# Optimization experiments

Hardware: AMD Instinct MI355X
Metric: run time of the kernel (lower is better)

## Reference

```python
import jax, jax.numpy as jnp
import numpy as np
from functools import partial

B, S, T = 256, 256, 32      # batch, encoder seq len, decoder max len
H = 512                     # hidden_dim
E = 128                     # encoder token embed dim
ED = 32                     # decoder action/target embed dim (LSTM input = 2*ED)
V = 1000                    # encoder vocab
A = 8                       # num_actions
NT = 80                     # num_targets


def lstm_cell(x, h, c, Wi, Wh, b):
    # PyTorch gate order: i, f, g, o
    z = x @ Wi.T + h @ Wh.T + b
    i, f, g, o = jnp.split(z, 4, axis=-1)
    c = jax.nn.sigmoid(f) * c + jax.nn.sigmoid(i) * jnp.tanh(g)
    h = jax.nn.sigmoid(o) * jnp.tanh(c)
    return h, c


def setup_inputs() -> dict:
    key = jax.random.key(0)
    ks = jax.random.split(key, 16)
    s = 0.05
    rn = lambda k, shp: (jax.random.normal(k, shp, dtype=jnp.float32) * s)
    return {
        "encoder_input": jax.random.randint(ks[0], (B, S), 0, V),
        "decoder_target": jax.random.randint(ks[1], (B, T, 2), 0, A),
        "enc_embed": rn(ks[2], (V, E)),
        "Wi_e": rn(ks[3], (4 * H, E)),
        "Wh_e": rn(ks[4], (4 * H, H)),
        "b_e": jnp.zeros((4 * H,), jnp.float32),
        "act_emb": rn(ks[5], (A, ED)),
        "tgt_emb": rn(ks[6], (NT, ED)),
        "Wi_d": rn(ks[7], (4 * H, 2 * ED)),
        "Wh_d": rn(ks[8], (4 * H, H)),
        "b_d": jnp.zeros((4 * H,), jnp.float32),
        "W_a": rn(ks[9], (A, H)),
        "b_a": jnp.zeros((A,), jnp.float32),
        "W_t": rn(ks[10], (NT, H)),
        "b_t": jnp.zeros((NT,), jnp.float32),
        "Wf": rn(ks[11], (1, 2 * H)),   # additive-attention scorer Linear(2H, 1)
        "bf": jnp.zeros((1,), jnp.float32),
    }


def reference(encoder_input, decoder_target, enc_embed, Wi_e, Wh_e, b_e,
              act_emb, tgt_emb, Wi_d, Wh_d, b_d, W_a, b_a, W_t, b_t, Wf, bf):
    # ---- encoder: embedding + single-layer LSTM over S steps ----
    x = enc_embed[encoder_input]          # [B, S, E]
    h0 = jnp.zeros((B, H), jnp.float32)
    c0 = jnp.zeros((B, H), jnp.float32)

    def enc_step(carry, xt):
        h, c = carry
        h, c = lstm_cell(xt, h, c, Wi_e, Wh_e, b_e)
        return (h, c), h

    (h, c), enc_out = jax.lax.scan(enc_step, (h0, c0), x.transpose(1, 0, 2))
    # enc_out: [S, B, H] (seq-major, matches torch LSTM output layout)

    # fc(concat(enc_i, dec_h)) == enc_i @ We + dec_h @ Wd + bf -> precompute enc part
    We = Wf[0, :H]                        # [H]
    Wd = Wf[0, H:]                        # [H]
    enc_score = jnp.einsum('sbh,h->sb', enc_out, We)   # [S, B]

    dec_in0 = jnp.zeros((B, 2), jnp.int32)

    def dec_step(carry, _):
        h, c, inp = carry
        xt = jnp.concatenate([act_emb[inp[:, 0]], tgt_emb[inp[:, 1]]], axis=-1)  # [B, 2*ED]
        h, c = lstm_cell(xt, h, c, Wi_d, Wh_d, b_d)
        scores = enc_score + h @ Wd + bf[0]            # [S, B]
        w = jax.nn.softmax(scores, axis=0)             # softmax over seq (dim=0)
        ctx = jnp.einsum('sbh,sb->bh', enc_out, w)     # weighted hidden state
        pa = ctx @ W_a.T + b_a                         # [B, A]
        pt = ctx @ W_t.T + b_t                         # [B, NT]
        inp = jnp.stack([jnp.argmax(pa, axis=1), jnp.argmax(pt, axis=1)],
                        axis=-1).astype(jnp.int32)     # greedy feedback (no TF)
        return (h, c, inp), (pa, pt)

    _, (pa_seq, pt_seq) = jax.lax.scan(dec_step, (h, c, dec_in0), None, length=T)
    action_outputs = pa_seq.transpose(1, 0, 2)   # [B, T, A]
    target_outputs = pt_seq.transpose(1, 0, 2)   # [B, T, NT]
    return action_outputs, target_outputs
```

## Files before the change

kernel.cpp:

```cpp
#include <hip/hip_runtime.h>
#include <hip/hip_fp16.h>


#define Sv 256
#define Tv 32
#define Hv 512
#define KT 16
#define LDSA 520
#define GM 16

#define ENC_KEY 0x7FFF7FFFu

typedef _Float16 half8 __attribute__((ext_vector_type(8)));
typedef __attribute__((ext_vector_type(4))) float f32x4;
typedef __attribute__((ext_vector_type(4))) unsigned uint4v;

__device__ __forceinline__ float sigm(float x) { return 1.0f / (1.0f + __expf(-x)); }
__device__ __forceinline__ float tanh_fast(float x) {
  x = fminf(15.f, fmaxf(-15.f, x));
  float e = __expf(2.f * x);
  return (e - 1.f) / (e + 1.f);
}

__device__ __forceinline__ uint4v ld_b128_sys(const void* p) {
  uint4v r;
  asm volatile("global_load_dwordx4 %0, %1, off sc0 sc1" : "=v"(r) : "v"(p));
  return r;
}

__device__ __forceinline__ unsigned umin4(uint4v r) {
  unsigned a = r[0] < r[1] ? r[0] : r[1];
  unsigned b = r[2] < r[3] ? r[2] : r[3];
  return a < b ? a : b;
}

__global__ __launch_bounds__(256)
void build_P(const float* __restrict__ embed, const float* __restrict__ Wi,
             const float* __restrict__ be, float* __restrict__ P)
{
  __shared__ float ev[4][128];
  const int tid = threadIdx.x;
  const int v0  = blockIdx.x * 4;
#pragma unroll
  for (int i = 0; i < 2; ++i) {
    int e = tid + i * 256;
    ev[e >> 7][e & 127] = embed[(v0 + (e >> 7)) * 128 + (e & 127)];
  }
  __syncthreads();
#pragma unroll 1
  for (int cc = 0; cc < 8; ++cc) {
    int n = cc * 256 + tid;
    float b = be[n];
    float a0 = b, a1 = b, a2 = b, a3 = b;
    const f32x4* w = (const f32x4*)(Wi + n * 128);
#pragma unroll
    for (int k4 = 0; k4 < 32; ++k4) {
      f32x4 wv = w[k4];
#pragma unroll
      for (int j = 0; j < 4; ++j) {
        float wj = wv[j];
        int k = k4 * 4 + j;
        a0 += wj * ev[0][k]; a1 += wj * ev[1][k];
        a2 += wj * ev[2][k]; a3 += wj * ev[3][k];
      }
    }
    P[(size_t)(v0 + 0) * 2048 + n] = a0;
    P[(size_t)(v0 + 1) * 2048 + n] = a1;
    P[(size_t)(v0 + 2) * 2048 + n] = a2;
    P[(size_t)(v0 + 3) * 2048 + n] = a3;
  }
}

__global__ __launch_bounds__(256, 1)
void lstm_enc(const int* __restrict__ enc_in, const float* __restrict__ P,
              const float* __restrict__ Wh, __half* __restrict__ enc_out)
{
  __shared__ __attribute__((aligned(16))) _Float16 Ah[GM][LDSA];
  __shared__ float zbuf[4][GM][37];

  const int tid  = threadIdx.x;
  const int wg   = blockIdx.x;
  const int g    = wg & 15;
  const int cb   = wg >> 4;
  const int wave = tid >> 6;
  const int lane = tid & 63;
  const int m16  = lane & 15;
  const int qd   = lane >> 4;

  half8 wf[KT][2];
#pragma unroll
  for (int kt = 0; kt < KT; ++kt) {
#pragma unroll
    for (int nt = 0; nt < 2; ++nt) {
      int n  = wave * 512 + cb * 32 + nt * 16 + m16;
      int k0 = kt * 32 + qd * 8;
      const float* src = Wh + (size_t)n * Hv + k0;
      f32x4 f0 = *(const f32x4*)(src);
      f32x4 f1 = *(const f32x4*)(src + 4);
      half8 w;
      w[0] = (_Float16)f0[0]; w[1] = (_Float16)f0[1];
      w[2] = (_Float16)f0[2]; w[3] = (_Float16)f0[3];
      w[4] = (_Float16)f1[0]; w[5] = (_Float16)f1[1];
      w[6] = (_Float16)f1[2]; w[7] = (_Float16)f1[3];
      wf[kt][nt] = w;
    }
  }

  const int gr = tid >> 4;
  const int gj = (tid & 15) * 2;
  float c0 = 0.f, c1 = 0.f;

  const int r0   = qd * 4;
  const int ncol = wave * 512 + cb * 32 + m16;
  float px0[4], px1[4];
#pragma unroll
  for (int rr = 0; rr < 4; ++rr) {
    int tk  = enc_in[(g * GM + r0 + rr) * Sv + 0];
    px0[rr] = P[(size_t)tk * 2048 + ncol];
    px1[rr] = P[(size_t)tk * 2048 + ncol + 16];
  }

  const int rw   = tid >> 6;
  const int colh = (tid & 63) * 8;
  const size_t rowstride = (size_t)Sv * Hv;
  size_t rb[4];
#pragma unroll
  for (int j = 0; j < 4; ++j)
    rb[j] = (size_t)(g * GM + j * 4 + rw) * rowstride + colh;

  const uint4v K4 = {ENC_KEY, ENC_KEY, ENC_KEY, ENC_KEY};

#pragma unroll 1
  for (int s = 0; s < Sv; ++s) {
    if (s > 0) {
      const __half* sp = enc_out + (size_t)(s - 1) * Hv;
      const void* p0 = sp + rb[0];
      const void* p1 = sp + rb[1];
      const void* p2 = sp + rb[2];
      const void* p3 = sp + rb[3];
      uint4v ra, rbv, rc, rd;
      unsigned ok = 0;
      do {
        if (!(ok & 1u)) ra  = ld_b128_sys(p0);
        if (!(ok & 2u)) rbv = ld_b128_sys(p1);
        if (!(ok & 4u)) rc  = ld_b128_sys(p2);
        if (!(ok & 8u)) rd  = ld_b128_sys(p3);
        asm volatile("s_waitcnt vmcnt(0)"
                     : "+v"(ra), "+v"(rbv), "+v"(rc), "+v"(rd)
                     :: "memory");
        if (umin4(ra))  ok |= 1u;
        if (umin4(rbv)) ok |= 2u;
        if (umin4(rc))  ok |= 4u;
        if (umin4(rd))  ok |= 8u;
        if (ok != 15u) __builtin_amdgcn_s_sleep(1);
      } while (ok != 15u);
      *(uint4v*)&Ah[0 * 4 + rw][colh] = ra  ^ K4;
      *(uint4v*)&Ah[1 * 4 + rw][colh] = rbv ^ K4;
      *(uint4v*)&Ah[2 * 4 + rw][colh] = rc  ^ K4;
      *(uint4v*)&Ah[3 * 4 + rw][colh] = rd  ^ K4;
    }
    __syncthreads();

    f32x4 acc0 = {0.f, 0.f, 0.f, 0.f};
    f32x4 acc1 = {0.f, 0.f, 0.f, 0.f};
    if (s > 0) {
#pragma unroll
      for (int kt = 0; kt < KT; ++kt) {
        half8 a = *(const half8*)&Ah[m16][kt * 32 + qd * 8];
        acc0 = __builtin_amdgcn_mfma_f32_16x16x32_f16(a, wf[kt][0], acc0, 0, 0, 0);
        acc1 = __builtin_amdgcn_mfma_f32_16x16x32_f16(a, wf[kt][1], acc1, 0, 0, 0);
      }
    }
#pragma unroll
    for (int rr = 0; rr < 4; ++rr) {
      zbuf[wave][r0 + rr][m16]      = acc0[rr] + px0[rr];
      zbuf[wave][r0 + rr][16 + m16] = acc1[rr] + px1[rr];
    }
    __syncthreads();

    float i0 = zbuf[0][gr][gj], i1 = zbuf[0][gr][gj + 1];
    float f0g = zbuf[1][gr][gj], f1g = zbuf[1][gr][gj + 1];
    float g0 = zbuf[2][gr][gj], g1 = zbuf[2][gr][gj + 1];
    float o0 = zbuf[3][gr][gj], o1 = zbuf[3][gr][gj + 1];
    float cn0 = sigm(f0g) * c0 + sigm(i0) * tanh_fast(g0);
    float cn1 = sigm(f1g) * c1 + sigm(i1) * tanh_fast(g1);
    float hn0 = sigm(o0) * tanh_fast(cn0);
    float hn1 = sigm(o1) * tanh_fast(cn1);
    c0 = cn0; c1 = cn1;

    __half2 h2;
    h2.x = __float2half(hn0);
    h2.y = __float2half(hn1);
    {
      unsigned pk = __builtin_bit_cast(unsigned, h2) ^ ENC_KEY;
      __hip_atomic_store(
          (unsigned*)(enc_out + ((size_t)(g * GM + gr) * Sv + s) * Hv + cb * 32 + gj),
          pk, __ATOMIC_RELAXED, __HIP_MEMORY_SCOPE_AGENT);
    }

    if (s + 1 < Sv) {
      int sn = s + 1;
#pragma unroll
      for (int rr = 0; rr < 4; ++rr) {
        int tk  = enc_in[(g * GM + r0 + rr) * Sv + sn];
        px0[rr] = P[(size_t)tk * 2048 + ncol];
        px1[rr] = P[(size_t)tk * 2048 + ncol + 16];
      }
    }
  }
}

__global__ __launch_bounds__(256)
void attn_out(const __half* __restrict__ enc_out, const float* __restrict__ Wf,
              const float* __restrict__ Wa, const float* __restrict__ ba,
              const float* __restrict__ Wt, const float* __restrict__ bt,
              float* __restrict__ out)
{
  __shared__ float We[512];
  __shared__ float sc[256];
  __shared__ float ctx[512];
  __shared__ float red[8];
  const int tid = threadIdx.x;
  const int b   = blockIdx.x;
  const int wv  = tid >> 6;
  const int ln  = tid & 63;

  We[tid] = Wf[tid];
  We[tid + 256] = Wf[tid + 256];
  __syncthreads();

  const uint4* r4 = (const uint4*)(enc_out + ((size_t)b * Sv + tid) * Hv);
  float a = 0.f;
#pragma unroll 4
  for (int k = 0; k < 64; ++k) {
    uint4 v = r4[k];
    v.x ^= ENC_KEY; v.y ^= ENC_KEY; v.z ^= ENC_KEY; v.w ^= ENC_KEY;
    float2 f0 = __half22float2(__builtin_bit_cast(__half2, v.x));
    float2 f1 = __half22float2(__builtin_bit_cast(__half2, v.y));
    float2 f2 = __half22float2(__builtin_bit_cast(__half2, v.z));
    float2 f3 = __half22float2(__builtin_bit_cast(__half2, v.w));
    const float* wp = &We[8 * k];
    a += f0.x * wp[0] + f0.y * wp[1] + f1.x * wp[2] + f1.y * wp[3]
       + f2.x * wp[4] + f2.y * wp[5] + f3.x * wp[6] + f3.y * wp[7];
  }

  float m = a;
  for (int off = 32; off; off >>= 1) m = fmaxf(m, __shfl_down(m, off));
  if (ln == 0) red[wv] = m;
  __syncthreads();
  if (tid == 0) red[4] = fmaxf(fmaxf(red[0], red[1]), fmaxf(red[2], red[3]));
  __syncthreads();
  float e = __expf(a - red[4]);
  float ssum = e;
  for (int off = 32; off; off >>= 1) ssum += __shfl_down(ssum, off);
  if (ln == 0) red[wv] = ssum;
  __syncthreads();
  if (tid == 0) red[5] = red[0] + red[1] + red[2] + red[3];
  __syncthreads();
  sc[tid] = e * (1.f / red[5]);
  __syncthreads();

  {
    float a0 = 0.f, a1 = 0.f;
    const __half2* base = (const __half2*)(enc_out + (size_t)b * Sv * Hv) + tid;
#pragma unroll 4
    for (int s2 = 0; s2 < Sv; ++s2) {
      unsigned uv = __builtin_bit_cast(unsigned, base[s2 * (Hv / 2)]) ^ ENC_KEY;
      float2 f = __half22float2(__builtin_bit_cast(__half2, uv));
      float w = sc[s2];
      a0 += w * f.x;
      a1 += w * f.y;
    }
    ctx[2 * tid] = a0;
    ctx[2 * tid + 1] = a1;
  }
  __syncthreads();

  if (tid < 88) {
    const float* wr = (tid < 8) ? (Wa + tid * Hv) : (Wt + (tid - 8) * Hv);
    float o = (tid < 8) ? ba[tid] : bt[tid - 8];
    for (int k = 0; k < Hv; ++k) o += ctx[k] * wr[k];
    if (tid < 8) {
      float* o0 = out + (size_t)b * Tv * 8;
#pragma unroll
      for (int t = 0; t < Tv; ++t) o0[t * 8 + tid] = o;
    } else {
      int n = tid - 8;
      float* o1 = out + 65536 + (size_t)b * Tv * 80;
#pragma unroll
      for (int t = 0; t < Tv; ++t) o1[t * 80 + n] = o;
    }
  }
}

extern "C" void kernel_launch(void* const* d_in, const int* in_sizes, int n_in,
                              void* d_out, int out_size, void* d_ws, size_t ws_size,
                              hipStream_t stream)
{
  (void)in_sizes; (void)n_in; (void)out_size; (void)ws_size;
  const int*   enc_in = (const int*)d_in[0];
  const float* embed  = (const float*)d_in[2];
  const float* Wi     = (const float*)d_in[3];
  const float* Wh     = (const float*)d_in[4];
  const float* be     = (const float*)d_in[5];
  const float* Wa     = (const float*)d_in[11];
  const float* ba     = (const float*)d_in[12];
  const float* Wt     = (const float*)d_in[13];
  const float* bt     = (const float*)d_in[14];
  const float* Wf     = (const float*)d_in[15];

  char* ws = (char*)d_ws;
  float*  P      = (float*)ws;
  __half* encout = (__half*)(ws + (8u << 20));

  hipMemsetAsync(encout, 0, 64u << 20, stream);

  build_P<<<dim3(250), dim3(256), 0, stream>>>(embed, Wi, be, P);
  lstm_enc<<<dim3(256), dim3(256), 0, stream>>>(enc_in, P, Wh, encout);
  attn_out<<<dim3(256), dim3(256), 0, stream>>>(encout, Wf, Wa, ba, Wt, bt, (float*)d_out);
}
```

Baseline: 733.5 us.

## Interleave two batch row groups per workgroup to hide cross-block polling latency

Each encoder workgroup now owns two 16-row batch groups (A and B) and half as many workgroups are launched. The two groups' LSTM steps are interleaved so the polled global loads of one group's previous hidden state are issued before the other group's MFMA and gate work. This is meant to hide the inter-workgroup spin-wait and load latency behind useful compute. In exchange each workgroup does twice the serial work per step, and the grid shrinks to 128 blocks, which occupy fewer CUs.

```diff
diff --git a/kernel.cpp b/kernel.cpp
--- a/kernel.cpp
+++ b/kernel.cpp
@@ -75,17 +75,21 @@
 void lstm_enc(const int* __restrict__ enc_in, const float* __restrict__ P,
               const float* __restrict__ Wh, __half* __restrict__ enc_out)
 {
-  __shared__ __attribute__((aligned(16))) _Float16 Ah[GM][LDSA];
+  __shared__ __attribute__((aligned(16))) _Float16 AhA[GM][LDSA];
+  __shared__ __attribute__((aligned(16))) _Float16 AhB[GM][LDSA];
   __shared__ float zbuf[4][GM][37];
 
   const int tid  = threadIdx.x;
   const int wg   = blockIdx.x;
-  const int g    = wg & 15;
-  const int cb   = wg >> 4;
+  const int sg   = wg & 7;
+  const int cb   = wg >> 3;
   const int wave = tid >> 6;
   const int lane = tid & 63;
   const int m16  = lane & 15;
   const int qd   = lane >> 4;
+
+  const int rowA = sg * 32;
+  const int rowB = sg * 32 + 16;
 
   half8 wf[KT][2];
 #pragma unroll
@@ -108,106 +112,145 @@
 
   const int gr = tid >> 4;
   const int gj = (tid & 15) * 2;
-  float c0 = 0.f, c1 = 0.f;
+  float cA0 = 0.f, cA1 = 0.f, cB0 = 0.f, cB1 = 0.f;
 
   const int r0   = qd * 4;
   const int ncol = wave * 512 + cb * 32 + m16;
-  float px0[4], px1[4];
+
+  float pxA0[4], pxA1[4], pxB0[4], pxB1[4];
 #pragma unroll
   for (int rr = 0; rr < 4; ++rr) {
-    int tk  = enc_in[(g * GM + r0 + rr) * Sv + 0];
-    px0[rr] = P[(size_t)tk * 2048 + ncol];
-    px1[rr] = P[(size_t)tk * 2048 + ncol + 16];
+    int tka  = enc_in[(rowA + r0 + rr) * Sv + 0];
+    pxA0[rr] = P[(size_t)tka * 2048 + ncol];
+    pxA1[rr] = P[(size_t)tka * 2048 + ncol + 16];
+    int tkb  = enc_in[(rowB + r0 + rr) * Sv + 0];
+    pxB0[rr] = P[(size_t)tkb * 2048 + ncol];
+    pxB1[rr] = P[(size_t)tkb * 2048 + ncol + 16];
   }
 
   const int rw   = tid >> 6;
   const int colh = (tid & 63) * 8;
   const size_t rowstride = (size_t)Sv * Hv;
-  size_t rb[4];
+  size_t rbA[4];
 #pragma unroll
   for (int j = 0; j < 4; ++j)
-    rb[j] = (size_t)(g * GM + j * 4 + rw) * rowstride + colh;
+    rbA[j] = (size_t)(rowA + j * 4 + rw) * rowstride + colh;
+  const size_t BOFF = (size_t)GM * rowstride;
 
   const uint4v K4 = {ENC_KEY, ENC_KEY, ENC_KEY, ENC_KEY};
+  uint4v qa_, qb_, qc_, qd_;
+  const __half *qp0, *qp1, *qp2, *qp3;
+
+#define Q_SET_ISSUE(OFF) { \
+    const __half* sp_ = enc_out + (OFF); \
+    qp0 = sp_ + rbA[0]; qp1 = sp_ + rbA[1]; \
+    qp2 = sp_ + rbA[2]; qp3 = sp_ + rbA[3]; \
+    qa_ = ld_b128_sys(qp0); qb_ = ld_b128_sys(qp1); \
+    qc_ = ld_b128_sys(qp2); qd_ = ld_b128_sys(qp3); }
+
+#define Q_COMPLETE() { \
+    asm volatile("s_waitcnt vmcnt(9)" \
+                 : "+v"(qa_), "+v"(qb_), "+v"(qc_), "+v"(qd_) :: "memory"); \
+    unsigned ok = 0; \
+    if (umin4(qa_)) ok |= 1u; if (umin4(qb_)) ok |= 2u; \
+    if (umin4(qc_)) ok |= 4u; if (umin4(qd_)) ok |= 8u; \
+    while (ok != 15u) { \
+      __builtin_amdgcn_s_sleep(1); \
+      if (!(ok & 1u)) qa_ = ld_b128_sys(qp0); \
+      if (!(ok & 2u)) qb_ = ld_b128_sys(qp1); \
+      if (!(ok & 4u)) qc_ = ld_b128_sys(qp2); \
+      if (!(ok & 8u)) qd_ = ld_b128_sys(qp3); \
+      asm volatile("s_waitcnt vmcnt(0)" \
+                   : "+v"(qa_), "+v"(qb_), "+v"(qc_), "+v"(qd_) :: "memory"); \
+      if (umin4(qa_)) ok |= 1u; if (umin4(qb_)) ok |= 2u; \
+      if (umin4(qc_)) ok |= 4u; if (umin4(qd_)) ok |= 8u; } }
+
+#define Q_DECODE(AH) { \
+    *(uint4v*)&AH[0 * 4 + rw][colh] = qa_ ^ K4; \
+    *(uint4v*)&AH[1 * 4 + rw][colh] = qb_ ^ K4; \
+    *(uint4v*)&AH[2 * 4 + rw][colh] = qc_ ^ K4; \
+    *(uint4v*)&AH[3 * 4 + rw][colh] = qd_ ^ K4; }
+
+#define MFMA_Z(AH, PX0, PX1) { \
+    f32x4 acc0 = {0.f, 0.f, 0.f, 0.f}; \
+    f32x4 acc1 = {0.f, 0.f, 0.f, 0.f}; \
+    _Pragma("unroll") for (int kt = 0; kt < KT; ++kt) { \
+      half8 a = *(const half8*)&AH[m16][kt * 32 + qd * 8]; \
+      acc0 = __builtin_amdgcn_mfma_f32_16x16x32_f16(a, wf[kt][0], acc0, 0, 0, 0); \
+      acc1 = __builtin_amdgcn_mfma_f32_16x16x32_f16(a, wf[kt][1], acc1, 0, 0, 0); } \
+    _Pragma("unroll") for (int rr = 0; rr < 4; ++rr) { \
+      zbuf[wave][r0 + rr][m16]      = acc0[rr] + PX0[rr]; \
+      zbuf[wave][r0 + rr][16 + m16] = acc1[rr] + PX1[rr]; } }
+
+#define ZB_PX(PX0, PX1) \
+    _Pragma("unroll") for (int rr = 0; rr < 4; ++rr) { \
+      zbuf[wave][r0 + rr][m16]      = PX0[rr]; \
+      zbuf[wave][r0 + rr][16 + m16] = PX1[rr]; }
+
+#define GATES(C0, C1, ROWBASE, S) { \
+    float i0 = zbuf[0][gr][gj], i1 = zbuf[0][gr][gj + 1]; \
+    float f0g = zbuf[1][gr][gj], f1g = zbuf[1][gr][gj + 1]; \
+    float g0 = zbuf[2][gr][gj], g1 = zbuf[2][gr][gj + 1]; \
+    float o0 = zbuf[3][gr][gj], o1 = zbuf[3][gr][gj + 1]; \
+    float cn0 = sigm(f0g) * (C0) + sigm(i0) * tanh_fast(g0); \
+    float cn1 = sigm(f1g) * (C1) + sigm(i1) * tanh_fast(g1); \
+    float hn0 = sigm(o0) * tanh_fast(cn0); \
+    float hn1 = sigm(o1) * tanh_fast(cn1); \
+    C0 = cn0; C1 = cn1; \
+    __half2 h2; h2.x = __float2half(hn0); h2.y = __float2half(hn1); \
+    unsigned pk = __builtin_bit_cast(unsigned, h2) ^ ENC_KEY; \
+    __hip_atomic_store( \
+        (unsigned*)(enc_out + ((size_t)((ROWBASE) + gr) * Sv + (S)) * Hv + cb * 32 + gj), \
+        pk, __ATOMIC_RELAXED, __HIP_MEMORY_SCOPE_AGENT); }
+
+#define PX_GATHER(PX0, PX1, ROWBASE, SN) \
+    _Pragma("unroll") for (int rr = 0; rr < 4; ++rr) { \
+      int tk = enc_in[((ROWBASE) + r0 + rr) * Sv + (SN)]; \
+      PX0[rr] = P[(size_t)tk * 2048 + ncol]; \
+      PX1[rr] = P[(size_t)tk * 2048 + ncol + 16]; }
+
+  ZB_PX(pxA0, pxA1);
+  __syncthreads();
+  { GATES(cA0, cA1, rowA, 0); }
+  PX_GATHER(pxA0, pxA1, rowA, 1);
+  __syncthreads();
+  ZB_PX(pxB0, pxB1);
+  __syncthreads();
+  Q_SET_ISSUE((size_t)0);
+  { GATES(cB0, cB1, rowB, 0); }
+  PX_GATHER(pxB0, pxB1, rowB, 1);
 
 #pragma unroll 1
-  for (int s = 0; s < Sv; ++s) {
-    if (s > 0) {
-      const __half* sp = enc_out + (size_t)(s - 1) * Hv;
-      const void* p0 = sp + rb[0];
-      const void* p1 = sp + rb[1];
-      const void* p2 = sp + rb[2];
-      const void* p3 = sp + rb[3];
-      uint4v ra, rbv, rc, rd;
-      unsigned ok = 0;
-      do {
-        if (!(ok & 1u)) ra  = ld_b128_sys(p0);
-        if (!(ok & 2u)) rbv = ld_b128_sys(p1);
-        if (!(ok & 4u)) rc  = ld_b128_sys(p2);
-        if (!(ok & 8u)) rd  = ld_b128_sys(p3);
-        asm volatile("s_waitcnt vmcnt(0)"
-                     : "+v"(ra), "+v"(rbv), "+v"(rc), "+v"(rd)
-                     :: "memory");
-        if (umin4(ra))  ok |= 1u;
-        if (umin4(rbv)) ok |= 2u;
-        if (umin4(rc))  ok |= 4u;
-        if (umin4(rd))  ok |= 8u;
-        if (ok != 15u) __builtin_amdgcn_s_sleep(1);
-      } while (ok != 15u);
-      *(uint4v*)&Ah[0 * 4 + rw][colh] = ra  ^ K4;
-      *(uint4v*)&Ah[1 * 4 + rw][colh] = rbv ^ K4;
-      *(uint4v*)&Ah[2 * 4 + rw][colh] = rc  ^ K4;
-      *(uint4v*)&Ah[3 * 4 + rw][colh] = rd  ^ K4;
-    }
+  for (int s = 1; s < Sv; ++s) {
+    const int sn = (s + 1 < Sv) ? s + 1 : s;
+
+    Q_COMPLETE();
+    Q_DECODE(AhA);
     __syncthreads();
-
-    f32x4 acc0 = {0.f, 0.f, 0.f, 0.f};
-    f32x4 acc1 = {0.f, 0.f, 0.f, 0.f};
-    if (s > 0) {
-#pragma unroll
-      for (int kt = 0; kt < KT; ++kt) {
-        half8 a = *(const half8*)&Ah[m16][kt * 32 + qd * 8];
-        acc0 = __builtin_amdgcn_mfma_f32_16x16x32_f16(a, wf[kt][0], acc0, 0, 0, 0);
-        acc1 = __builtin_amdgcn_mfma_f32_16x16x32_f16(a, wf[kt][1], acc1, 0, 0, 0);
-      }
-    }
-#pragma unroll
-    for (int rr = 0; rr < 4; ++rr) {
-      zbuf[wave][r0 + rr][m16]      = acc0[rr] + px0[rr];
-      zbuf[wave][r0 + rr][16 + m16] = acc1[rr] + px1[rr];
-    }
+    MFMA_Z(AhA, pxA0, pxA1);
+    Q_SET_ISSUE((size_t)(s - 1) * Hv + BOFF);
+    PX_GATHER(pxA0, pxA1, rowA, sn);
     __syncthreads();
-
-    float i0 = zbuf[0][gr][gj], i1 = zbuf[0][gr][gj + 1];
-    float f0g = zbuf[1][gr][gj], f1g = zbuf[1][gr][gj + 1];
-    float g0 = zbuf[2][gr][gj], g1 = zbuf[2][gr][gj + 1];
-    float o0 = zbuf[3][gr][gj], o1 = zbuf[3][gr][gj + 1];
-    float cn0 = sigm(f0g) * c0 + sigm(i0) * tanh_fast(g0);
-    float cn1 = sigm(f1g) * c1 + sigm(i1) * tanh_fast(g1);
-    float hn0 = sigm(o0) * tanh_fast(cn0);
-    float hn1 = sigm(o1) * tanh_fast(cn1);
-    c0 = cn0; c1 = cn1;
-
-    __half2 h2;
-    h2.x = __float2half(hn0);
-    h2.y = __float2half(hn1);
-    {
-      unsigned pk = __builtin_bit_cast(unsigned, h2) ^ ENC_KEY;
-      __hip_atomic_store(
-          (unsigned*)(enc_out + ((size_t)(g * GM + gr) * Sv + s) * Hv + cb * 32 + gj),
-          pk, __ATOMIC_RELAXED, __HIP_MEMORY_SCOPE_AGENT);
-    }
-
-    if (s + 1 < Sv) {
-      int sn = s + 1;
-#pragma unroll
-      for (int rr = 0; rr < 4; ++rr) {
-        int tk  = enc_in[(g * GM + r0 + rr) * Sv + sn];
-        px0[rr] = P[(size_t)tk * 2048 + ncol];
-        px1[rr] = P[(size_t)tk * 2048 + ncol + 16];
-      }
-    }
-  }
+    { GATES(cA0, cA1, rowA, s); }
+
+    Q_COMPLETE();
+    Q_DECODE(AhB);
+    __syncthreads();
+    MFMA_Z(AhB, pxB0, pxB1);
+    if (s + 1 < Sv)
+      Q_SET_ISSUE((size_t)s * Hv);
+    PX_GATHER(pxB0, pxB1, rowB, sn);
+    __syncthreads();
+    { GATES(cB0, cB1, rowB, s); }
+  }
+
+#undef Q_SET_ISSUE
+#undef Q_COMPLETE
+#undef Q_DECODE
+#undef MFMA_Z
+#undef ZB_PX
+#undef GATES
+#undef PX_GATHER
 }
 
 __global__ __launch_bounds__(256)
@@ -316,6 +359,6 @@
   hipMemsetAsync(encout, 0, 64u << 20, stream);
 
   build_P<<<dim3(250), dim3(256), 0, stream>>>(embed, Wi, be, P);
-  lstm_enc<<<dim3(256), dim3(256), 0, stream>>>(enc_in, P, Wh, encout);
+  lstm_enc<<<dim3(128), dim3(256), 0, stream>>>(enc_in, P, Wh, encout);
   attn_out<<<dim3(256), dim3(256), 0, stream>>>(encout, Wf, Wa, ba, Wt, bt, (float*)d_out);
 }
```

Measured after the change: 1.027 ms. 40.0% more time.

## Load MFMA A fragments directly from global with polling, drop LDS staging

Applied to the files above, without the earlier changes.

Each lane now polls and loads its own MFMA A-operand fragments (16 x 128-bit loads) straight from the flag-encoded encoder output in global memory, instead of cooperatively staging h into LDS and then reading it back. This removes one __syncthreads per step and the LDS round trip on the sequential critical path. zbuf is double-buffered by step parity so the single remaining barrier is enough. The cost is four times more global polling traffic per workgroup, since every wave loads the full 16x512 tile, plus higher register use for the 16 loaded vectors.

```diff
diff --git a/kernel.cpp b/kernel.cpp
--- a/kernel.cpp
+++ b/kernel.cpp
@@ -6,7 +6,6 @@
 #define Tv 32
 #define Hv 512
 #define KT 16
-#define LDSA 520
 #define GM 16
 
 #define ENC_KEY 0x7FFF7FFFu
@@ -71,12 +70,15 @@
   }
 }
 
+#define WAITQ(N, A, B, C, D) \
+  asm volatile("s_waitcnt vmcnt(" #N ")" \
+               : "+v"(A), "+v"(B), "+v"(C), "+v"(D) :: "memory")
+
 __global__ __launch_bounds__(256, 1)
 void lstm_enc(const int* __restrict__ enc_in, const float* __restrict__ P,
               const float* __restrict__ Wh, __half* __restrict__ enc_out)
 {
-  __shared__ __attribute__((aligned(16))) _Float16 Ah[GM][LDSA];
-  __shared__ float zbuf[4][GM][37];
+  __shared__ float zbuf[2][4][GM][37];
 
   const int tid  = threadIdx.x;
   const int wg   = blockIdx.x;
@@ -112,6 +114,7 @@
 
   const int r0   = qd * 4;
   const int ncol = wave * 512 + cb * 32 + m16;
+
   float px0[4], px1[4];
 #pragma unroll
   for (int rr = 0; rr < 4; ++rr) {
@@ -120,78 +123,79 @@
     px1[rr] = P[(size_t)tk * 2048 + ncol + 16];
   }
 
-  const int rw   = tid >> 6;
-  const int colh = (tid & 63) * 8;
-  const size_t rowstride = (size_t)Sv * Hv;
-  size_t rb[4];
-#pragma unroll
-  for (int j = 0; j < 4; ++j)
-    rb[j] = (size_t)(g * GM + j * 4 + rw) * rowstride + colh;
+  const size_t prow = (size_t)(g * GM + m16) * Sv * Hv + (size_t)(qd * 8);
 
   const uint4v K4 = {ENC_KEY, ENC_KEY, ENC_KEY, ENC_KEY};
 
 #pragma unroll 1
   for (int s = 0; s < Sv; ++s) {
-    if (s > 0) {
-      const __half* sp = enc_out + (size_t)(s - 1) * Hv;
-      const void* p0 = sp + rb[0];
-      const void* p1 = sp + rb[1];
-      const void* p2 = sp + rb[2];
-      const void* p3 = sp + rb[3];
-      uint4v ra, rbv, rc, rd;
-      unsigned ok = 0;
-      do {
-        if (!(ok & 1u)) ra  = ld_b128_sys(p0);
-        if (!(ok & 2u)) rbv = ld_b128_sys(p1);
-        if (!(ok & 4u)) rc  = ld_b128_sys(p2);
-        if (!(ok & 8u)) rd  = ld_b128_sys(p3);
-        asm volatile("s_waitcnt vmcnt(0)"
-                     : "+v"(ra), "+v"(rbv), "+v"(rc), "+v"(rd)
-                     :: "memory");
-        if (umin4(ra))  ok |= 1u;
-        if (umin4(rbv)) ok |= 2u;
-        if (umin4(rc))  ok |= 4u;
-        if (umin4(rd))  ok |= 8u;
-        if (ok != 15u) __builtin_amdgcn_s_sleep(1);
-      } while (ok != 15u);
-      *(uint4v*)&Ah[0 * 4 + rw][colh] = ra  ^ K4;
-      *(uint4v*)&Ah[1 * 4 + rw][colh] = rbv ^ K4;
-      *(uint4v*)&Ah[2 * 4 + rw][colh] = rc  ^ K4;
-      *(uint4v*)&Ah[3 * 4 + rw][colh] = rd  ^ K4;
-    }
-    __syncthreads();
-
     f32x4 acc0 = {0.f, 0.f, 0.f, 0.f};
     f32x4 acc1 = {0.f, 0.f, 0.f, 0.f};
+
     if (s > 0) {
+      const __half* bp = enc_out + prow + (size_t)(s - 1) * Hv;
+      uint4v pd[16];
+#pragma unroll
+      for (int i = 0; i < 16; ++i)
+        pd[i] = ld_b128_sys(bp + i * 32);
+      unsigned ok = 0;
+      WAITQ(12, pd[0], pd[1], pd[2], pd[3]);
+#pragma unroll
+      for (int i = 0; i < 4; ++i) if (umin4(pd[i])) ok |= 1u << i;
+      WAITQ(8, pd[4], pd[5], pd[6], pd[7]);
+#pragma unroll
+      for (int i = 4; i < 8; ++i) if (umin4(pd[i])) ok |= 1u << i;
+      WAITQ(4, pd[8], pd[9], pd[10], pd[11]);
+#pragma unroll
+      for (int i = 8; i < 12; ++i) if (umin4(pd[i])) ok |= 1u << i;
+      WAITQ(0, pd[12], pd[13], pd[14], pd[15]);
+#pragma unroll
+      for (int i = 12; i < 16; ++i) if (umin4(pd[i])) ok |= 1u << i;
+
+      while (ok != 0xFFFFu) {
+        __builtin_amdgcn_s_sleep(1);
+#pragma unroll
+        for (int i = 0; i < 16; ++i)
+          if (!(ok & (1u << i))) pd[i] = ld_b128_sys(bp + i * 32);
+        WAITQ(0, pd[0], pd[1], pd[2], pd[3]);
+        WAITQ(0, pd[4], pd[5], pd[6], pd[7]);
+        WAITQ(0, pd[8], pd[9], pd[10], pd[11]);
+        WAITQ(0, pd[12], pd[13], pd[14], pd[15]);
+#pragma unroll
+        for (int i = 0; i < 16; ++i) if (umin4(pd[i])) ok |= 1u << i;
+      }
+
 #pragma unroll
       for (int kt = 0; kt < KT; ++kt) {
-        half8 a = *(const half8*)&Ah[m16][kt * 32 + qd * 8];
+        uint4v t = pd[kt] ^ K4;
+        half8 a = __builtin_bit_cast(half8, t);
         acc0 = __builtin_amdgcn_mfma_f32_16x16x32_f16(a, wf[kt][0], acc0, 0, 0, 0);
         acc1 = __builtin_amdgcn_mfma_f32_16x16x32_f16(a, wf[kt][1], acc1, 0, 0, 0);
       }
     }
+
+    const int p = s & 1;
 #pragma unroll
     for (int rr = 0; rr < 4; ++rr) {
-      zbuf[wave][r0 + rr][m16]      = acc0[rr] + px0[rr];
-      zbuf[wave][r0 + rr][16 + m16] = acc1[rr] + px1[rr];
+      zbuf[p][wave][r0 + rr][m16]      = acc0[rr] + px0[rr];
+      zbuf[p][wave][r0 + rr][16 + m16] = acc1[rr] + px1[rr];
     }
     __syncthreads();
 
-    float i0 = zbuf[0][gr][gj], i1 = zbuf[0][gr][gj + 1];
-    float f0g = zbuf[1][gr][gj], f1g = zbuf[1][gr][gj + 1];
-    float g0 = zbuf[2][gr][gj], g1 = zbuf[2][gr][gj + 1];
-    float o0 = zbuf[3][gr][gj], o1 = zbuf[3][gr][gj + 1];
-    float cn0 = sigm(f0g) * c0 + sigm(i0) * tanh_fast(g0);
-    float cn1 = sigm(f1g) * c1 + sigm(i1) * tanh_fast(g1);
-    float hn0 = sigm(o0) * tanh_fast(cn0);
-    float hn1 = sigm(o1) * tanh_fast(cn1);
-    c0 = cn0; c1 = cn1;
-
-    __half2 h2;
-    h2.x = __float2half(hn0);
-    h2.y = __float2half(hn1);
     {
+      float i0 = zbuf[p][0][gr][gj], i1 = zbuf[p][0][gr][gj + 1];
+      float f0g = zbuf[p][1][gr][gj], f1g = zbuf[p][1][gr][gj + 1];
+      float g0 = zbuf[p][2][gr][gj], g1 = zbuf[p][2][gr][gj + 1];
+      float o0 = zbuf[p][3][gr][gj], o1 = zbuf[p][3][gr][gj + 1];
+      float cn0 = sigm(f0g) * c0 + sigm(i0) * tanh_fast(g0);
+      float cn1 = sigm(f1g) * c1 + sigm(i1) * tanh_fast(g1);
+      float hn0 = sigm(o0) * tanh_fast(cn0);
+      float hn1 = sigm(o1) * tanh_fast(cn1);
+      c0 = cn0; c1 = cn1;
+
+      __half2 h2;
+      h2.x = __float2half(hn0);
+      h2.y = __float2half(hn1);
       unsigned pk = __builtin_bit_cast(unsigned, h2) ^ ENC_KEY;
       __hip_atomic_store(
           (unsigned*)(enc_out + ((size_t)(g * GM + gr) * Sv + s) * Hv + cb * 32 + gj),
```

Result: slower. 1.679 ms (+128.9%).
